# Kernel tuning notes

Measured on AMD Instinct MI355X. Metric: run time of the kernel, lower is better.

The kernel has to match this reference:

```python
import jax, jax.numpy as jnp
import numpy as np
from jax import lax

DIM = 256


def _lstm_scan(x_tbd, lengths, W, b, c0, h0):
    """Masked LSTM over time. x_tbd: [T,B,D]. CudnnCompatible gate order i,g,f,o, forget_bias=0.
    Returns final (c, h) with states frozen at t >= lengths (dynamic_rnn semantics)."""
    T = x_tbd.shape[0]

    def step(carry, inp):
        c, h = carry
        xt, t = inp
        gates = jnp.concatenate([xt, h], axis=-1) @ W + b  # [B, 4D]
        i, g, f, o = jnp.split(gates, 4, axis=-1)
        c_new = jax.nn.sigmoid(f) * c + jax.nn.sigmoid(i) * jnp.tanh(g)
        h_new = jnp.tanh(c_new) * jax.nn.sigmoid(o)
        mask = (t < lengths)[:, None]
        c = jnp.where(mask, c_new, c)
        h = jnp.where(mask, h_new, h)
        y = jnp.where(mask, h_new, jnp.zeros_like(h_new))
        return (c, h), y

    (c, h), ys = lax.scan(step, (c0, h0), (x_tbd, jnp.arange(T)))
    return c, h, ys


def _reverse_seq(x, lengths):
    """tf.reverse_sequence along time axis 1: reverse first lengths[b] steps, keep the rest."""
    T = x.shape[1]
    t = jnp.arange(T)[None, :]
    L = lengths[:, None]
    idx = jnp.where(t < L, L - 1 - t, t)  # [B, T]
    return jnp.take_along_axis(x, idx[:, :, None], axis=1)


def setup_inputs() -> dict:
    key = jax.random.key(0)
    ks = jax.random.split(key, 12)
    B, T, D = 64, 512, DIM
    x = jax.random.normal(ks[0], (B, T, D), dtype=jnp.float32)
    length = jax.random.randint(ks[1], (B,), 1, T + 1, dtype=jnp.int32)
    scale = 1.0 / np.sqrt(2 * D)
    W_f = jax.random.normal(ks[2], (2 * D, 4 * D), dtype=jnp.float32) * scale
    b_f = jnp.zeros((4 * D,), dtype=jnp.float32)
    W_b = jax.random.normal(ks[3], (2 * D, 4 * D), dtype=jnp.float32) * scale
    b_b = jnp.zeros((4 * D,), dtype=jnp.float32)
    c_init_f = jax.random.normal(ks[4], (1, D), dtype=jnp.float32) * 0.01
    h_init_f = jax.random.normal(ks[5], (1, D), dtype=jnp.float32) * 0.01
    c_init_b = jax.random.normal(ks[6], (1, D), dtype=jnp.float32) * 0.01
    h_init_b = jax.random.normal(ks[7], (1, D), dtype=jnp.float32) * 0.01
    W_fc = jax.random.normal(ks[8], (2 * D, D), dtype=jnp.float32) * (1.0 / np.sqrt(2 * D))
    return {"x": x, "length": length, "W_f": W_f, "b_f": b_f, "W_b": W_b, "b_b": b_b,
            "c_init_f": c_init_f, "h_init_f": h_init_f, "c_init_b": c_init_b,
            "h_init_b": h_init_b, "W_fc": W_fc}


def reference(x, length, W_f, b_f, W_b, b_b, c_init_f, h_init_f, c_init_b, h_init_b, W_fc):
    B = x.shape[0]
    c0_f = jnp.tile(c_init_f, (B, 1))
    h0_f = jnp.tile(h_init_f, (B, 1))
    c0_b = jnp.tile(c_init_b, (B, 1))
    h0_b = jnp.tile(h_init_b, (B, 1))
    x_tbd = jnp.swapaxes(x, 0, 1)  # [T,B,D]
    _, h_f, _ = _lstm_scan(x_tbd, length, W_f, b_f, c0_f, h0_f)
    x_rev = jnp.swapaxes(_reverse_seq(x, length), 0, 1)
    _, h_b, _ = _lstm_scan(x_rev, length, W_b, b_b, c0_b, h0_b)
    # return_seq=False: concat final hidden states and project (no bias)
    return jnp.concatenate([h_f, h_b], axis=-1) @ W_fc
```

## Files before the change

### kernel.cpp

```cpp
#include <hip/hip_runtime.h>

#define T_STEPS 512
#define BATCH   64
#define DIMS    256
#define NBLK    16
#define NDIR    2

typedef short bf16x8 __attribute__((ext_vector_type(8)));
typedef float f32x4  __attribute__((ext_vector_type(4)));

__device__ __forceinline__ unsigned short f2bf(float f) {
  union { float f; unsigned int u; } v; v.f = f;
  unsigned int b = v.u;
  return (unsigned short)((b + 0x7FFFu + ((b >> 16) & 1u)) >> 16);
}

__device__ __forceinline__ float sigm(float x) {
  return __builtin_amdgcn_rcpf(1.0f + __builtin_amdgcn_exp2f(-1.44269504f * x));
}
__device__ __forceinline__ float tanh_(float x) {
  return 1.0f - 2.0f * __builtin_amdgcn_rcpf(1.0f + __builtin_amdgcn_exp2f(2.88539008f * x));
}

__device__ __forceinline__ f32x4 bcast4(float s) {
  f32x4 v; v[0] = s; v[1] = s; v[2] = s; v[3] = s; return v;
}

__global__ void prep_x(const float* __restrict__ x, unsigned short* __restrict__ xbf) {
  size_t i = ((size_t)blockIdx.x * 256 + threadIdx.x) * 4;
  const float4 v = *reinterpret_cast<const float4*>(x + i);
  uint2 o;
  o.x = (unsigned)f2bf(v.x) | ((unsigned)f2bf(v.y) << 16);
  o.y = (unsigned)f2bf(v.z) | ((unsigned)f2bf(v.w) << 16);
  *reinterpret_cast<uint2*>(xbf + i) = o;
}

__global__ void prep_w(const float* __restrict__ Wf, const float* __restrict__ Wb,
                       unsigned short* __restrict__ WT) {
  int d = blockIdx.x >> 10, col = blockIdx.x & 1023;
  const float* W = d ? Wb : Wf;
  int k = threadIdx.x;
  WT[((size_t)(d * 1024 + col)) * 512 + k] = f2bf(W[(size_t)k * 1024 + col]);
}

__global__ __launch_bounds__(256, 1) void lstm_rec(
    const unsigned short* __restrict__ xbf,
    const unsigned short* __restrict__ WT,
    const float* __restrict__ bias_f, const float* __restrict__ bias_b,
    const float* __restrict__ ci_f, const float* __restrict__ hi_f,
    const float* __restrict__ ci_b, const float* __restrict__ hi_b,
    const int* __restrict__ length,
    unsigned short* hbuf,
    float* hfinal,
    int* counters)
{
  const int blk = blockIdx.x;
  const int d = blk >> 4, g = blk & 15;
  const int lane = threadIdx.x & 63;
  const int wv = threadIdx.x >> 6;
  const int lhi = lane >> 4, llo = lane & 15;

  const float* bias = d ? bias_b : bias_f;
  const float* cini = d ? ci_b : ci_f;
  const float* hini = d ? hi_b : hi_f;
  unsigned short* hb = hbuf + (size_t)d * (2 * BATCH * DIMS);
  int* cnt = counters + (d * 4 + wv) * 16;

  const int dim = g * 16 + llo;

  bf16x8 wf[4][16];
  #pragma unroll
  for (int gate = 0; gate < 4; ++gate) {
    #pragma unroll
    for (int ks = 0; ks < 16; ++ks) {
      const unsigned short* p =
          WT + ((size_t)(d * 1024 + gate * 256 + dim)) * 512 + ks * 32 + lhi * 8;
      wf[gate][ks] = *reinterpret_cast<const bf16x8*>(p);
      asm volatile("" : "+v"(wf[gate][ks]));
    }
  }
  float bs[4];
  #pragma unroll
  for (int gate = 0; gate < 4; ++gate) bs[gate] = bias[gate * 256 + dim];

  const int b0 = wv * 16 + lhi * 4;
  float c[4], h[4];
  int Ld[4];
  #pragma unroll
  for (int j = 0; j < 4; ++j) {
    c[j] = cini[dim]; h[j] = hini[dim]; Ld[j] = length[b0 + j];
  }

  const int bx = wv * 16 + llo;
  const int Lx = length[bx];

  #pragma unroll
  for (int j = 0; j < 4; ++j)
    __hip_atomic_store(&hb[(b0 + j) * DIMS + dim], f2bf(h[j]),
                       __ATOMIC_RELAXED, __HIP_MEMORY_SCOPE_AGENT);
  if (lane == 0)
    __hip_atomic_fetch_add(cnt, 1, __ATOMIC_RELEASE, __HIP_MEMORY_SCOPE_AGENT);

  bf16x8 xa[8];
  {
    const int tx0 = (d == 0) ? 0 : (Lx - 1);
    const unsigned short* xp = xbf + ((size_t)bx * T_STEPS + tx0) * DIMS + lhi * 8;
    #pragma unroll
    for (int ks = 0; ks < 8; ++ks) xa[ks] = *reinterpret_cast<const bf16x8*>(xp + ks * 32);
  }

  #pragma unroll 1
  for (int t = 0; t < T_STEPS; ++t) {
    f32x4 acc[4];
    #pragma unroll
    for (int gate = 0; gate < 4; ++gate) acc[gate] = bcast4(bs[gate]);

    #pragma unroll
    for (int ks = 0; ks < 8; ++ks) {
      #pragma unroll
      for (int gate = 0; gate < 4; ++gate)
        acc[gate] = __builtin_amdgcn_mfma_f32_16x16x32_bf16(xa[ks], wf[gate][ks], acc[gate], 0, 0, 0);
    }

    {
      const int target = 16 * (t + 1);
      while (__hip_atomic_load(cnt, __ATOMIC_RELAXED, __HIP_MEMORY_SCOPE_AGENT) < target) {}
    }

    const unsigned short* hrd =
        hb + (size_t)(t & 1) * (BATCH * DIMS) + bx * DIMS + lhi * 8;
    bf16x8 ha[8];
    #pragma unroll
    for (int ks = 0; ks < 8; ++ks)
      asm volatile("global_load_dwordx4 %0, %1, off sc0 sc1"
                   : "=v"(ha[ks]) : "v"(hrd + ks * 32) : "memory");
    asm volatile("s_waitcnt vmcnt(0)" ::: "memory");
    __builtin_amdgcn_sched_barrier(0);

    if (t + 1 < T_STEPS) {
      const int tn = t + 1;
      const int tx = (d == 0) ? tn : ((tn < Lx) ? (Lx - 1 - tn) : tn);
      const unsigned short* xp = xbf + ((size_t)bx * T_STEPS + tx) * DIMS + lhi * 8;
      #pragma unroll
      for (int ks = 0; ks < 8; ++ks) xa[ks] = *reinterpret_cast<const bf16x8*>(xp + ks * 32);
    }

    #pragma unroll
    for (int ks = 0; ks < 8; ++ks) {
      #pragma unroll
      for (int gate = 0; gate < 4; ++gate)
        acc[gate] = __builtin_amdgcn_mfma_f32_16x16x32_bf16(ha[ks], wf[gate][ks + 8], acc[gate], 0, 0, 0);
    }

    unsigned short* hw = hb + (size_t)((t + 1) & 1) * (BATCH * DIMS);
    #pragma unroll
    for (int j = 0; j < 4; ++j) {
      const float gi = acc[0][j], gg = acc[1][j], gf = acc[2][j], go = acc[3][j];
      const float cn = sigm(gf) * c[j] + sigm(gi) * tanh_(gg);
      const float hn = tanh_(cn) * sigm(go);
      if (t < Ld[j]) { c[j] = cn; h[j] = hn; }
      __hip_atomic_store(&hw[(b0 + j) * DIMS + dim], f2bf(h[j]),
                         __ATOMIC_RELAXED, __HIP_MEMORY_SCOPE_AGENT);
    }

    if (lane == 0)
      __hip_atomic_fetch_add(cnt, 1, __ATOMIC_RELEASE, __HIP_MEMORY_SCOPE_AGENT);
  }

  #pragma unroll
  for (int j = 0; j < 4; ++j)
    hfinal[((size_t)d * BATCH + b0 + j) * DIMS + dim] = h[j];
}

__global__ void final_gemm(const float* __restrict__ hfinal, const float* __restrict__ Wfc,
                           float* __restrict__ out) {
  __shared__ float hrow[512];
  const int b = blockIdx.x, col = threadIdx.x;
  hrow[col]       = hfinal[(size_t)b * DIMS + col];
  hrow[256 + col] = hfinal[(size_t)(BATCH + b) * DIMS + col];
  __syncthreads();
  float acc = 0.f;
  #pragma unroll 8
  for (int k = 0; k < 512; ++k) acc = fmaf(hrow[k], Wfc[(size_t)k * DIMS + col], acc);
  out[(size_t)b * DIMS + col] = acc;
}

extern "C" void kernel_launch(void* const* d_in, const int* in_sizes, int n_in,
                              void* d_out, int out_size, void* d_ws, size_t ws_size,
                              hipStream_t stream) {
  const float* x        = (const float*)d_in[0];
  const int*   length   = (const int*)d_in[1];
  const float* W_f      = (const float*)d_in[2];
  const float* b_f      = (const float*)d_in[3];
  const float* W_b      = (const float*)d_in[4];
  const float* b_b      = (const float*)d_in[5];
  const float* c_init_f = (const float*)d_in[6];
  const float* h_init_f = (const float*)d_in[7];
  const float* c_init_b = (const float*)d_in[8];
  const float* h_init_b = (const float*)d_in[9];
  const float* W_fc     = (const float*)d_in[10];
  float* out = (float*)d_out;

  char* ws = (char*)d_ws;
  unsigned short* xbf = (unsigned short*)(ws);
  unsigned short* WT  = (unsigned short*)(ws + 16777216);
  unsigned short* hbf = (unsigned short*)(ws + 16777216 + 2097152);
  float* hfinal       = (float*)(ws + 16777216 + 2097152 + 131072);
  int*   counters     = (int*)(ws + 16777216 + 2097152 + 131072 + 131072);

  hipMemsetAsync(counters, 0, NDIR * 4 * 16 * sizeof(int), stream);
  prep_x<<<8192, 256, 0, stream>>>(x, xbf);
  prep_w<<<2048, 512, 0, stream>>>(W_f, W_b, WT);
  lstm_rec<<<NBLK * NDIR, 256, 0, stream>>>(xbf, WT, b_f, b_b,
                                            c_init_f, h_init_f, c_init_b, h_init_b,
                                            length, hbf, hfinal, counters);
  final_gemm<<<BATCH, 256, 0, stream>>>(hfinal, W_fc, out);
}
```

Before: 2.451 ms.

## Replace counter barrier with per-element step tags packed alongside bf16 hidden states

Removes the per-wave atomic counter and spin-wait. Each hidden-state element is stored as a 32-bit word holding a step tag in the high half and the bf16 value in the low half. Readers poll the h buffer until every tag matches the current step, then unpack the bf16 values. This drops one release-atomic round trip and a separate polling load per step, but doubles the bytes each h read moves and adds unpack ALU work. The h buffer is now memset to zero instead of the counters.

Result: faster. 2.094 ms (-14.6%).

```diff
diff --git a/kernel.cpp b/kernel.cpp
--- a/kernel.cpp
+++ b/kernel.cpp
@@ -8,6 +8,7 @@
 
 typedef short bf16x8 __attribute__((ext_vector_type(8)));
 typedef float f32x4  __attribute__((ext_vector_type(4)));
+typedef unsigned int u32x4 __attribute__((ext_vector_type(4)));
 
 __device__ __forceinline__ unsigned short f2bf(float f) {
   union { float f; unsigned int u; } v; v.f = f;
@@ -50,9 +51,8 @@
     const float* __restrict__ ci_f, const float* __restrict__ hi_f,
     const float* __restrict__ ci_b, const float* __restrict__ hi_b,
     const int* __restrict__ length,
-    unsigned short* hbuf,
-    float* hfinal,
-    int* counters)
+    unsigned int* hbuf,
+    float* hfinal)
 {
   const int blk = blockIdx.x;
   const int d = blk >> 4, g = blk & 15;
@@ -63,8 +63,7 @@
   const float* bias = d ? bias_b : bias_f;
   const float* cini = d ? ci_b : ci_f;
   const float* hini = d ? hi_b : hi_f;
-  unsigned short* hb = hbuf + (size_t)d * (2 * BATCH * DIMS);
-  int* cnt = counters + (d * 4 + wv) * 16;
+  unsigned int* hb = hbuf + (size_t)d * (2 * BATCH * DIMS);
 
   const int dim = g * 16 + llo;
 
@@ -95,11 +94,12 @@
   const int Lx = length[bx];
 
   #pragma unroll
-  for (int j = 0; j < 4; ++j)
-    __hip_atomic_store(&hb[(b0 + j) * DIMS + dim], f2bf(h[j]),
-                       __ATOMIC_RELAXED, __HIP_MEMORY_SCOPE_AGENT);
-  if (lane == 0)
-    __hip_atomic_fetch_add(cnt, 1, __ATOMIC_RELEASE, __HIP_MEMORY_SCOPE_AGENT);
+  for (int j = 0; j < 4; ++j) {
+    unsigned int val = (1u << 16) | (unsigned int)f2bf(h[j]);
+    const unsigned int* ap = hb + (b0 + j) * DIMS + dim;
+    asm volatile("global_store_dword %0, %1, off sc0 sc1"
+                 :: "v"(ap), "v"(val) : "memory");
+  }
 
   bf16x8 xa[8];
   {
@@ -122,20 +122,42 @@
         acc[gate] = __builtin_amdgcn_mfma_f32_16x16x32_bf16(xa[ks], wf[gate][ks], acc[gate], 0, 0, 0);
     }
 
+    const unsigned int* hr = hb + (size_t)(t & 1) * (BATCH * DIMS) + bx * DIMS + lhi * 8;
+    u32x4 w[16];
     {
-      const int target = 16 * (t + 1);
-      while (__hip_atomic_load(cnt, __ATOMIC_RELAXED, __HIP_MEMORY_SCOPE_AGENT) < target) {}
-    }
-
-    const unsigned short* hrd =
-        hb + (size_t)(t & 1) * (BATCH * DIMS) + bx * DIMS + lhi * 8;
+      const unsigned int tagsh = (unsigned int)(t + 1) << 16;
+      bool ready;
+      do {
+        #pragma unroll
+        for (int ks = 0; ks < 8; ++ks) {
+          const unsigned int* p = hr + ks * 32;
+          asm volatile("global_load_dwordx4 %0, %1, off sc0 sc1"
+                       : "=v"(w[2 * ks]) : "v"(p) : "memory");
+          asm volatile("global_load_dwordx4 %0, %1, off sc0 sc1"
+                       : "=v"(w[2 * ks + 1]) : "v"(p + 4) : "memory");
+        }
+        asm volatile("s_waitcnt vmcnt(0)" ::: "memory");
+        unsigned int bad = 0;
+        #pragma unroll
+        for (int i = 0; i < 16; ++i)
+          #pragma unroll
+          for (int q = 0; q < 4; ++q)
+            bad |= (w[i][q] ^ tagsh);
+        ready = ((bad >> 16) == 0);
+      } while (!__all(ready));
+    }
+    __builtin_amdgcn_sched_barrier(0);
+
     bf16x8 ha[8];
     #pragma unroll
-    for (int ks = 0; ks < 8; ++ks)
-      asm volatile("global_load_dwordx4 %0, %1, off sc0 sc1"
-                   : "=v"(ha[ks]) : "v"(hrd + ks * 32) : "memory");
-    asm volatile("s_waitcnt vmcnt(0)" ::: "memory");
-    __builtin_amdgcn_sched_barrier(0);
+    for (int ks = 0; ks < 8; ++ks) {
+      union { bf16x8 v; unsigned int dd[4]; } u;
+      u.dd[0] = (w[2 * ks][0]     & 0xFFFFu) | (w[2 * ks][1]     << 16);
+      u.dd[1] = (w[2 * ks][2]     & 0xFFFFu) | (w[2 * ks][3]     << 16);
+      u.dd[2] = (w[2 * ks + 1][0] & 0xFFFFu) | (w[2 * ks + 1][1] << 16);
+      u.dd[3] = (w[2 * ks + 1][2] & 0xFFFFu) | (w[2 * ks + 1][3] << 16);
+      ha[ks] = u.v;
+    }
 
     if (t + 1 < T_STEPS) {
       const int tn = t + 1;
@@ -152,19 +174,19 @@
         acc[gate] = __builtin_amdgcn_mfma_f32_16x16x32_bf16(ha[ks], wf[gate][ks + 8], acc[gate], 0, 0, 0);
     }
 
-    unsigned short* hw = hb + (size_t)((t + 1) & 1) * (BATCH * DIMS);
+    unsigned int* hw = hb + (size_t)((t + 1) & 1) * (BATCH * DIMS);
+    const unsigned int ptag = (unsigned int)(t + 2) << 16;
     #pragma unroll
     for (int j = 0; j < 4; ++j) {
       const float gi = acc[0][j], gg = acc[1][j], gf = acc[2][j], go = acc[3][j];
       const float cn = sigm(gf) * c[j] + sigm(gi) * tanh_(gg);
       const float hn = tanh_(cn) * sigm(go);
       if (t < Ld[j]) { c[j] = cn; h[j] = hn; }
-      __hip_atomic_store(&hw[(b0 + j) * DIMS + dim], f2bf(h[j]),
-                         __ATOMIC_RELAXED, __HIP_MEMORY_SCOPE_AGENT);
-    }
-
-    if (lane == 0)
-      __hip_atomic_fetch_add(cnt, 1, __ATOMIC_RELEASE, __HIP_MEMORY_SCOPE_AGENT);
+      unsigned int val = ptag | (unsigned int)f2bf(h[j]);
+      const unsigned int* ap = hw + (b0 + j) * DIMS + dim;
+      asm volatile("global_store_dword %0, %1, off sc0 sc1"
+                   :: "v"(ap), "v"(val) : "memory");
+    }
   }
 
   #pragma unroll
@@ -204,15 +226,14 @@
   char* ws = (char*)d_ws;
   unsigned short* xbf = (unsigned short*)(ws);
   unsigned short* WT  = (unsigned short*)(ws + 16777216);
-  unsigned short* hbf = (unsigned short*)(ws + 16777216 + 2097152);
-  float* hfinal       = (float*)(ws + 16777216 + 2097152 + 131072);
-  int*   counters     = (int*)(ws + 16777216 + 2097152 + 131072 + 131072);
-
-  hipMemsetAsync(counters, 0, NDIR * 4 * 16 * sizeof(int), stream);
+  unsigned int*   hbf = (unsigned int*)(ws + 16777216 + 2097152);
+  float* hfinal       = (float*)(ws + 16777216 + 2097152 + 524288);
+
+  hipMemsetAsync(hbf, 0, NDIR * 2 * BATCH * DIMS * sizeof(unsigned int), stream);
   prep_x<<<8192, 256, 0, stream>>>(x, xbf);
   prep_w<<<2048, 512, 0, stream>>>(W_f, W_b, WT);
   lstm_rec<<<NBLK * NDIR, 256, 0, stream>>>(xbf, WT, b_f, b_b,
                                             c_init_f, h_init_f, c_init_b, h_init_b,
-                                            length, hbf, hfinal, counters);
+                                            length, hbf, hfinal);
   final_gemm<<<BATCH, 256, 0, stream>>>(hfinal, W_fc, out);
 }
```
